# Kernel optimization log

Measured on AMD Instinct MI355X. Metric: run time of the kernel, lower is better.

Reference implementation:

```python
import jax, jax.numpy as jnp
import numpy as np
from jax import lax


def setup_inputs() -> dict:
    key = jax.random.key(0)
    # [C=512, H=256, W=256] feature map
    x = jax.random.normal(key, (512, 256, 256), dtype=jnp.float32)
    return {"x": x}


def reference(x):
    # Original torch forward mutates x in place: _bottom_pool (cummax down rows,
    # axis=1) modifies x and returns it, then _right_pool (cummax across cols,
    # axis=2) runs on the SAME already-bottom-pooled tensor. Thus `bottom` and
    # `right` alias and out = 2 * cummax_w(cummax_h(x)).
    y = lax.cummax(lax.cummax(x, axis=1), axis=2)
    return y + y
```

## Files before the change

### kernel.cpp

```cpp
#include <hip/hip_runtime.h>
#include <math.h>

#define CC 512
#define HH 256
#define WW 256
#define RB 64
#define NT 256

__global__ __launch_bounds__(NT) void corner_pool_kernel(const float* __restrict__ x,
                                                         float* __restrict__ out) {
    __shared__ float tile[RB][WW];
    const int c    = blockIdx.x;
    const int t    = threadIdx.x;
    const int lane = t & 63;
    const int wave = t >> 6;

    const float* xc = x   + (size_t)c * HH * WW;
    float*       oc = out + (size_t)c * HH * WW;

    float cm = -INFINITY;

    for (int rb = 0; rb < HH / RB; ++rb) {
        const float* src = xc + rb * RB * WW;
        #pragma unroll
        for (int i = 0; i < (RB * WW) / (NT * 4); ++i) {
            int j   = i * NT + t;
            int row = j >> 6;
            int c4  = j & 63;
            float4 v = *(const float4*)(src + row * WW + c4 * 4);
            *(float4*)&tile[row][c4 * 4] = v;
        }
        __syncthreads();

        #pragma unroll 8
        for (int r = 0; r < RB; ++r) {
            float v = tile[r][t];
            cm = fmaxf(cm, v);
            tile[r][t] = cm;
        }
        __syncthreads();

        #pragma unroll 4
        for (int rr = 0; rr < RB / 4; ++rr) {
            int r = wave * (RB / 4) + rr;
            float4 v = *(const float4*)&tile[r][lane * 4];
            float p0 = v.x;
            float p1 = fmaxf(p0, v.y);
            float p2 = fmaxf(p1, v.z);
            float p3 = fmaxf(p2, v.w);
            float s = p3;
            #pragma unroll
            for (int d = 1; d < 64; d <<= 1) {
                float u = __shfl_up(s, d);
                if (lane >= d) s = fmaxf(s, u);
            }
            float e = __shfl_up(s, 1);
            if (lane == 0) e = -INFINITY;
            float4 o;
            o.x = 2.0f * fmaxf(e, p0);
            o.y = 2.0f * fmaxf(e, p1);
            o.z = 2.0f * fmaxf(e, p2);
            o.w = 2.0f * fmaxf(e, p3);
            *(float4*)(oc + (size_t)(rb * RB + r) * WW + lane * 4) = o;
        }
        __syncthreads();
    }
}

extern "C" void kernel_launch(void* const* d_in, const int* in_sizes, int n_in,
                              void* d_out, int out_size, void* d_ws, size_t ws_size,
                              hipStream_t stream) {
    const float* x = (const float*)d_in[0];
    float* out = (float*)d_out;
    corner_pool_kernel<<<dim3(CC), dim3(NT), 0, stream>>>(x, out);
}
```

Before: 49.78 us.

## Double-buffer row tiles with async global-to-LDS loads and DPP wave scan

Replaces the synchronous global-to-register-to-LDS tile load with global_load_lds directly into a double-buffered LDS tile, so the next 32-row tile is prefetched while the current one is scanned. The cross-lane prefix max is rewritten with DPP row-shift and row-broadcast operations instead of shfl_up, output stores become nontemporal, and raw s_barrier/s_waitcnt replace __syncthreads. This aims to hide global load latency and cut shuffle overhead, at the cost of fragile manual wait counts and DPP correctness that depends on the wave64 row layout.

```diff
diff --git a/kernel.cpp b/kernel.cpp
--- a/kernel.cpp
+++ b/kernel.cpp
@@ -4,66 +4,102 @@
 #define CC 512
 #define HH 256
 #define WW 256
-#define RB 64
+#define RB 32
+#define NTILES (HH / RB)
 #define NT 256
+#define RPW (RB / 4)
+
+typedef float f32x4 __attribute__((ext_vector_type(4)));
+
+#define BAR()    asm volatile("s_barrier" ::: "memory")
+#define WAITV(N) asm volatile("s_waitcnt vmcnt(" #N ")" ::: "memory")
+#define WAITL()  asm volatile("s_waitcnt lgkmcnt(0)" ::: "memory")
+
+template<int CTRL, int ROW_MASK>
+__device__ __forceinline__ float dpp_ninf(float v) {
+    union { float f; int i; } o, s, r;
+    o.f = -INFINITY;
+    s.f = v;
+    r.i = __builtin_amdgcn_update_dpp(o.i, s.i, CTRL, ROW_MASK, 0xF, false);
+    return r.f;
+}
+
+__device__ __forceinline__ float wave_incl_max(float v) {
+    v = fmaxf(v, dpp_ninf<0x111, 0xF>(v));
+    v = fmaxf(v, dpp_ninf<0x112, 0xF>(v));
+    v = fmaxf(v, dpp_ninf<0x114, 0xF>(v));
+    v = fmaxf(v, dpp_ninf<0x118, 0xF>(v));
+    v = fmaxf(v, dpp_ninf<0x142, 0xA>(v));
+    v = fmaxf(v, dpp_ninf<0x143, 0xC>(v));
+    return v;
+}
+
+__device__ __forceinline__ void stage_rows(const float* src, float* lds_row_base,
+                                           int wave, int lane) {
+    #pragma unroll
+    for (int i = 0; i < RPW; ++i) {
+        int r = wave * RPW + i;
+        const float* g = src + r * WW + lane * 4;
+        __builtin_amdgcn_global_load_lds(
+            (const __attribute__((address_space(1))) void*)g,
+            (__attribute__((address_space(3))) void*)(lds_row_base + r * WW),
+            16, 0, 0);
+    }
+}
 
 __global__ __launch_bounds__(NT) void corner_pool_kernel(const float* __restrict__ x,
                                                          float* __restrict__ out) {
-    __shared__ float tile[RB][WW];
-    const int c    = blockIdx.x;
+    __shared__ float tile[2][RB][WW];
     const int t    = threadIdx.x;
     const int lane = t & 63;
     const int wave = t >> 6;
+    const int c    = blockIdx.x;
 
     const float* xc = x   + (size_t)c * HH * WW;
     float*       oc = out + (size_t)c * HH * WW;
 
     float cm = -INFINITY;
 
-    for (int rb = 0; rb < HH / RB; ++rb) {
-        const float* src = xc + rb * RB * WW;
+    stage_rows(xc, &tile[0][0][0], wave, lane);
+
+    #pragma unroll
+    for (int ti = 0; ti < NTILES; ++ti) {
+        const int cb = ti & 1;
+
+        if (ti + 1 < NTILES) {
+            stage_rows(xc + (size_t)(ti + 1) * RB * WW, &tile[cb ^ 1][0][0], wave, lane);
+            WAITV(8);
+        } else {
+            WAITV(0);
+        }
+        BAR();
+
         #pragma unroll
-        for (int i = 0; i < (RB * WW) / (NT * 4); ++i) {
-            int j   = i * NT + t;
-            int row = j >> 6;
-            int c4  = j & 63;
-            float4 v = *(const float4*)(src + row * WW + c4 * 4);
-            *(float4*)&tile[row][c4 * 4] = v;
+        for (int r = 0; r < RB; ++r) {
+            cm = fmaxf(cm, tile[cb][r][t]);
+            tile[cb][r][t] = cm;
         }
-        __syncthreads();
+        WAITL();
+        BAR();
 
-        #pragma unroll 8
-        for (int r = 0; r < RB; ++r) {
-            float v = tile[r][t];
-            cm = fmaxf(cm, v);
-            tile[r][t] = cm;
-        }
-        __syncthreads();
-
-        #pragma unroll 4
-        for (int rr = 0; rr < RB / 4; ++rr) {
-            int r = wave * (RB / 4) + rr;
-            float4 v = *(const float4*)&tile[r][lane * 4];
+        #pragma unroll
+        for (int i = 0; i < RPW; ++i) {
+            int r = wave * RPW + i;
+            f32x4 v = *(const f32x4*)&tile[cb][r][lane * 4];
             float p0 = v.x;
             float p1 = fmaxf(p0, v.y);
             float p2 = fmaxf(p1, v.z);
             float p3 = fmaxf(p2, v.w);
-            float s = p3;
-            #pragma unroll
-            for (int d = 1; d < 64; d <<= 1) {
-                float u = __shfl_up(s, d);
-                if (lane >= d) s = fmaxf(s, u);
-            }
-            float e = __shfl_up(s, 1);
-            if (lane == 0) e = -INFINITY;
-            float4 o;
+            float s  = wave_incl_max(p3);
+            float e  = dpp_ninf<0x138, 0xF>(s);
+            f32x4 o;
             o.x = 2.0f * fmaxf(e, p0);
             o.y = 2.0f * fmaxf(e, p1);
             o.z = 2.0f * fmaxf(e, p2);
             o.w = 2.0f * fmaxf(e, p3);
-            *(float4*)(oc + (size_t)(rb * RB + r) * WW + lane * 4) = o;
+            __builtin_nontemporal_store(o, (f32x4*)(oc + (size_t)(ti * RB + r) * WW + lane * 4));
         }
-        __syncthreads();
+        BAR();
     }
 }
 
```

Result: faster. 46.94 us (-5.7%).
